# Optimization experiments

Measured on AMD Instinct MI355X. Metric: run time of the kernel, lower is better.

The kernel has to match this reference:

```python
import jax, jax.numpy as jnp
import numpy as np

DIM = 2048
NUM_SLOTS = 64
MEM_DIM = 512
TEMP = 0.1


def setup_inputs() -> dict:
    key = jax.random.key(0)
    k_x, k_mem, k_kp, k_vp, k_gw, k_gb = jax.random.split(key, 6)
    B, L = 8, 4096
    return {
        "x": jax.random.normal(k_x, (B, L, DIM), dtype=jnp.float32),
        "memory": jax.random.normal(k_mem, (NUM_SLOTS, MEM_DIM), dtype=jnp.float32),
        # torch Linear weight layout: [out_features, in_features]
        "key_w": jax.random.normal(k_kp, (MEM_DIM, DIM), dtype=jnp.float32) * (1.0 / np.sqrt(DIM)),
        "value_w": jax.random.normal(k_vp, (DIM, MEM_DIM), dtype=jnp.float32) * (1.0 / np.sqrt(MEM_DIM)),
        "gate_w": jax.random.normal(k_gw, (1, 2 * DIM), dtype=jnp.float32) * (1.0 / np.sqrt(2 * DIM)),
        "gate_b": jnp.zeros((1,), dtype=jnp.float32),
    }


def reference(x, memory, key_w, value_w, gate_w, gate_b):
    # query = key_proj(x): [B,L,mem_dim]
    query = jnp.einsum('bld,md->blm', x, key_w)
    # attention over memory slots: [B,L,num_slots]
    attn = jax.nn.softmax(jnp.einsum('blm,nm->bln', query, memory) / TEMP, axis=-1)
    # retrieve and project back to dim: [B,L,dim]
    retrieved = jnp.einsum('bln,nm->blm', attn, memory)
    retrieved = jnp.einsum('blm,dm->bld', retrieved, value_w)
    # gate from concat([x, retrieved]) -> Linear(2*dim, 1) -> sigmoid
    gate_logit = (jnp.einsum('bld,od->blo', x, gate_w[:, :DIM])
                  + jnp.einsum('bld,od->blo', retrieved, gate_w[:, DIM:])
                  + gate_b)
    gate = jax.nn.sigmoid(gate_logit)  # [B,L,1]
    return gate * x + (1.0 - gate) * retrieved
```

## Files before the change

### kernel.cpp

```cpp
#include <hip/hip_runtime.h>
#include <stdint.h>

#define DIM   2048
#define NSLOT 64
#define MDIM  512
#define TINV  10.0f

typedef __attribute__((ext_vector_type(4))) float     f32x4;
typedef __attribute__((ext_vector_type(8))) _Float16  half8;

#define MFMA16(a,b,c) __builtin_amdgcn_mfma_f32_16x16x32_f16((a),(b),(c),0,0,0)

#define OFF_W2F   0
#define OFF_W3T   1310720
#define OFF_H     1572864
#define OFF_TPART 1573120

__device__ __forceinline__ size_t w2f_idx(int row, int k, int lvl) {
    const int t  = row >> 4, ar = row & 15;
    const int ch = k >> 7, ks = (k >> 5) & 3, kg = (k >> 3) & 3, e = k & 7;
    return ((size_t)((((ch * 5 + t) * 4 + ks) * 2 + lvl) * 64) + kg * 16 + ar) * 8 + e;
}


__global__ __launch_bounds__(256) void prep_all(
    const float* __restrict__ memory, const float* __restrict__ key_w,
    const float* __restrict__ value_w, const float* __restrict__ gate_w,
    _Float16* __restrict__ W2F, _Float16* __restrict__ W3T,
    float* __restrict__ tpart)
{
    const int tid = threadIdx.x;
    const int c = blockIdx.x;
    const int role = blockIdx.y;

    if (role == 17) {
        const int b = c;
        float a0 = 0.f, a1 = 0.f;
        for (int d = b * 256; d < b * 256 + 256; ++d) {
            const float gv = gate_w[DIM + d];
            a0 = fmaf(value_w[(size_t)d * MDIM + tid], gv, a0);
            a1 = fmaf(value_w[(size_t)d * MDIM + tid + 256], gv, a1);
        }
        tpart[b * 512 + tid] = a0;
        tpart[b * 512 + tid + 256] = a1;
        return;
    }

    if (role < 9) {
        const int g = role;
        const int k = c * 256 + tid;
        if (g == 8) {
            float v = gate_w[k];
            _Float16 ph = (_Float16)v;
            _Float16 pl = (_Float16)(v - (float)ph);
            W2F[w2f_idx(64, k, 0)] = ph;
            W2F[w2f_idx(64, k, 1)] = pl;
            for (int r = 65; r < 80; ++r) {
                W2F[w2f_idx(r, k, 0)] = (_Float16)0.f;
                W2F[w2f_idx(r, k, 1)] = (_Float16)0.f;
            }
            return;
        }
        __shared__ __align__(16) float mem_s[8 * MDIM];
        for (int i = tid; i < 8 * MDIM; i += 256)
            mem_s[i] = memory[g * 8 * MDIM + i];
        __syncthreads();

        const f32x4* ms4 = (const f32x4*)mem_s;
        float acc[8] = {};
        for (int m4 = 0; m4 < MDIM / 4; ++m4) {
            const float kw0 = key_w[(size_t)(m4 * 4 + 0) * DIM + k];
            const float kw1 = key_w[(size_t)(m4 * 4 + 1) * DIM + k];
            const float kw2 = key_w[(size_t)(m4 * 4 + 2) * DIM + k];
            const float kw3 = key_w[(size_t)(m4 * 4 + 3) * DIM + k];
            #pragma unroll
            for (int i = 0; i < 8; ++i) {
                const f32x4 mv = ms4[i * (MDIM / 4) + m4];
                acc[i] = fmaf(mv.x, kw0, acc[i]);
                acc[i] = fmaf(mv.y, kw1, acc[i]);
                acc[i] = fmaf(mv.z, kw2, acc[i]);
                acc[i] = fmaf(mv.w, kw3, acc[i]);
            }
        }
        #pragma unroll
        for (int i = 0; i < 8; ++i) {
            float v = acc[i];
            _Float16 ph = (_Float16)v;
            _Float16 pl = (_Float16)(v - (float)ph);
            W2F[w2f_idx(g * 8 + i, k, 0)] = ph;
            W2F[w2f_idx(g * 8 + i, k, 1)] = pl;
        }
        return;
    }

    {
        const int g = role - 9;
        const int d = c * 256 + tid;
        __shared__ __align__(16) float mem_s2[8 * MDIM];
        for (int i = tid; i < 8 * MDIM; i += 256)
            mem_s2[i] = memory[g * 8 * MDIM + i];
        __syncthreads();

        const f32x4* ms4 = (const f32x4*)mem_s2;
        const f32x4* vp = (const f32x4*)(value_w + (size_t)d * MDIM);
        float acc[8] = {};
        for (int m4 = 0; m4 < MDIM / 4; ++m4) {
            const f32x4 v = vp[m4];
            #pragma unroll
            for (int i = 0; i < 8; ++i) {
                const f32x4 mv = ms4[i * (MDIM / 4) + m4];
                acc[i] = fmaf(mv.x, v.x, acc[i]);
                acc[i] = fmaf(mv.y, v.y, acc[i]);
                acc[i] = fmaf(mv.z, v.z, acc[i]);
                acc[i] = fmaf(mv.w, v.w, acc[i]);
            }
        }
        #pragma unroll
        for (int i = 0; i < 8; ++i)
            W3T[(size_t)d * NSLOT + g * 8 + i] = (_Float16)acc[i];
    }
}

__global__ __launch_bounds__(512) void prep_h(
    const float* __restrict__ memory, const float* __restrict__ tpart,
    float* __restrict__ h)
{
    __shared__ float ts[512];
    const int tid = threadIdx.x;
    float s = 0.f;
    #pragma unroll
    for (int b = 0; b < 8; ++b) s += tpart[b * 512 + tid];
    ts[tid] = s;
    __syncthreads();
    const int lane = tid & 63, w = tid >> 6;
    #pragma unroll
    for (int q = 0; q < 8; ++q) {
        const int n = w * 8 + q;
        float p = 0.f;
        for (int m = lane; m < MDIM; m += 64)
            p = fmaf(memory[(size_t)n * MDIM + m], ts[m], p);
        #pragma unroll
        for (int off = 32; off; off >>= 1) p += __shfl_xor(p, off);
        if (lane == 0) h[n] = p;
    }
}


__global__ __launch_bounds__(512, 4) void fused_kernel(
    const float* __restrict__ x,
    const _Float16* __restrict__ W2F,
    const _Float16* __restrict__ W3T,
    const float* __restrict__ h, const float* __restrict__ gate_b,
    float* __restrict__ out)
{
    __shared__ __align__(16) float ppart[4 * 5 * 64 * 4];
    __shared__ __align__(16) _Float16 attn_s[4][16][72];
    __shared__ float gate_s[4][16];

    const int tid  = threadIdx.x;
    const int lane = tid & 63;
    const int w    = tid >> 6;
    const int mt   = w & 3;
    const int kh   = w >> 2;
    const int arow = lane & 15;
    const int kg   = lane >> 4;
    const size_t row0 = (size_t)blockIdx.x * 64;

    f32x4 acc[5];
    {   f32x4 z = {0.f, 0.f, 0.f, 0.f};
        #pragma unroll
        for (int t = 0; t < 5; ++t) acc[t] = z; }

    const float* xrow = x + (row0 + mt * 16 + arow) * DIM + kg * 8;
    const _Float16* w2l8 = W2F + lane * 8;
    const int chbase = kh * 8;

    f32x4 xA[8], xB[8];
    auto load_x = [&](f32x4* X, int chn) {
        #pragma unroll
        for (int ks = 0; ks < 4; ++ks) {
            X[ks * 2]     = *(const f32x4*)(xrow + chn * 128 + ks * 32);
            X[ks * 2 + 1] = *(const f32x4*)(xrow + chn * 128 + ks * 32 + 4);
        }
    };
    auto compute_chunk = [&](const f32x4* X, int ch) {
        #pragma unroll
        for (int ks = 0; ks < 4; ++ks) {
            const f32x4 xa = X[ks * 2];
            const f32x4 xb = X[ks * 2 + 1];
            const float xf[8] = {xa.x, xa.y, xa.z, xa.w, xb.x, xb.y, xb.z, xb.w};
            _Float16 hh[8], ll[8];
            #pragma unroll
            for (int u = 0; u < 8; ++u) {
                hh[u] = (_Float16)xf[u];
                ll[u] = (_Float16)(xf[u] - (float)hh[u]);
            }
            const half8 ah = {hh[0], hh[1], hh[2], hh[3], hh[4], hh[5], hh[6], hh[7]};
            const half8 al = {ll[0], ll[1], ll[2], ll[3], ll[4], ll[5], ll[6], ll[7]};
            #pragma unroll
            for (int t = 0; t < 5; ++t) {
                const _Float16* p = w2l8 + (size_t)(((ch * 5 + t) * 4 + ks) * 2) * 512;
                const half8 bh = *(const half8*)p;
                const half8 bl = *(const half8*)(p + 512);
                acc[t] = MFMA16(ah, bh, acc[t]);
                acc[t] = MFMA16(al, bh, acc[t]);
                acc[t] = MFMA16(ah, bl, acc[t]);
            }
        }
    };

    load_x(xA, chbase);
    for (int cp = 0; cp < 8; cp += 2) {
        load_x(xB, chbase + cp + 1);
        compute_chunk(xA, chbase + cp);
        if (cp + 2 < 8) load_x(xA, chbase + cp + 2);
        compute_chunk(xB, chbase + cp + 1);
    }

    if (kh == 1) {
        #pragma unroll
        for (int t = 0; t < 5; ++t)
            *(f32x4*)(ppart + (size_t)((mt * 5 + t) * 64 + lane) * 4) = acc[t];
    }
    __syncthreads();

    if (kh == 0) {
        #pragma unroll
        for (int t = 0; t < 5; ++t)
            acc[t] += *(const f32x4*)(ppart + (size_t)((mt * 5 + t) * 64 + lane) * 4);

        float hl[4];
        #pragma unroll
        for (int t = 0; t < 4; ++t) hl[t] = h[t * 16 + arow];
        const float gb = gate_b[0];

        #pragma unroll
        for (int j = 0; j < 4; ++j) {
            float m = fmaxf(fmaxf(acc[0][j], acc[1][j]), fmaxf(acc[2][j], acc[3][j]));
            #pragma unroll
            for (int off = 1; off < 16; off <<= 1) m = fmaxf(m, __shfl_xor(m, off));
            float p[4];
            float sum = 0.f;
            #pragma unroll
            for (int t = 0; t < 4; ++t) { p[t] = __expf((acc[t][j] - m) * TINV); sum += p[t]; }
            #pragma unroll
            for (int off = 1; off < 16; off <<= 1) sum += __shfl_xor(sum, off);
            const float inv = 1.f / sum;
            float gp = 0.f;
            #pragma unroll
            for (int t = 0; t < 4; ++t) {
                const float a = p[t] * inv;
                attn_s[mt][kg * 4 + j][t * 16 + arow] = (_Float16)a;
                gp = fmaf(a, hl[t], gp);
            }
            #pragma unroll
            for (int off = 1; off < 16; off <<= 1) gp += __shfl_xor(gp, off);
            const float sg = __shfl(acc[4][j], lane & 48);
            if (arow == 0)
                gate_s[mt][kg * 4 + j] = 1.f / (1.f + __expf(-(sg + gp + gb)));
        }
    }
    __syncthreads();

    const size_t rbase = row0 + mt * 16;
    const half8 a0 = *(const half8*)(&attn_s[mt][arow][kg * 8]);
    const half8 a1 = *(const half8*)(&attn_s[mt][arow][kg * 8 + 32]);
    const float g = gate_s[mt][arow];

    const size_t rowoff = (rbase + arow) * DIM + kh * 1024 + kg * 4;
    const float* xp = x + rowoff;
    float* op = out + rowoff;
    const _Float16* w3base = W3T + (size_t)(kh * 1024 + arow) * NSLOT + kg * 8;

    half8 qb0[4], qb1[4];
    f32x4 qx[4];
    #pragma unroll
    for (int s = 0; s < 4; ++s) {
        const _Float16* bp = w3base + (size_t)s * 16 * NSLOT;
        qb0[s] = *(const half8*)bp;
        qb1[s] = *(const half8*)(bp + 32);
        qx[s]  = *(const f32x4*)(xp + s * 16);
    }

    #pragma unroll 4
    for (int dt = 0; dt < 64; ++dt) {
        const int s = dt & 3;
        f32x4 r = {0.f, 0.f, 0.f, 0.f};
        r = MFMA16(qb0[s], a0, r);
        r = MFMA16(qb1[s], a1, r);
        const f32x4 xv = qx[s];
        int nt = dt + 4; if (nt > 63) nt = 63;
        const _Float16* bp = w3base + (size_t)nt * 16 * NSLOT;
        qb0[s] = *(const half8*)bp;
        qb1[s] = *(const half8*)(bp + 32);
        qx[s]  = *(const f32x4*)(xp + (size_t)nt * 16);
        f32x4 o;
        o.x = fmaf(g, xv.x - r.x, r.x);
        o.y = fmaf(g, xv.y - r.y, r.y);
        o.z = fmaf(g, xv.z - r.z, r.z);
        o.w = fmaf(g, xv.w - r.w, r.w);
        *(f32x4*)(op + dt * 16) = o;
    }
}


extern "C" void kernel_launch(void* const* d_in, const int* in_sizes, int n_in,
                              void* d_out, int out_size, void* d_ws, size_t ws_size,
                              hipStream_t stream) {
    (void)in_sizes; (void)n_in; (void)out_size; (void)ws_size;
    const float* x       = (const float*)d_in[0];
    const float* memory  = (const float*)d_in[1];
    const float* key_w   = (const float*)d_in[2];
    const float* value_w = (const float*)d_in[3];
    const float* gate_w  = (const float*)d_in[4];
    const float* gate_b  = (const float*)d_in[5];
    float* out = (float*)d_out;

    char* wsb = (char*)d_ws;
    _Float16* W2F = (_Float16*)(wsb + OFF_W2F);
    _Float16* W3T = (_Float16*)(wsb + OFF_W3T);
    float*    h   = (float*)(wsb + OFF_H);
    float*    tpt = (float*)(wsb + OFF_TPART);

    prep_all<<<dim3(8, 18), 256, 0, stream>>>(memory, key_w, value_w, gate_w,
                                              W2F, W3T, tpt);
    prep_h  <<<1, 512, 0, stream>>>(memory, tpt, h);

    fused_kernel<<<512, 512, 0, stream>>>(x, W2F, W3T, h, gate_b, out);
}
```

Measured before the change: 301.5 us.

## Stage W2 chunks in LDS via async global_load_lds and split K by ks

```diff
diff --git a/kernel.cpp b/kernel.cpp
--- a/kernel.cpp
+++ b/kernel.cpp
@@ -153,6 +153,7 @@
     const float* __restrict__ h, const float* __restrict__ gate_b,
     float* __restrict__ out)
 {
+    __shared__ __align__(16) _Float16 w2s[20480];
     __shared__ __align__(16) float ppart[4 * 5 * 64 * 4];
     __shared__ __align__(16) _Float16 attn_s[4][16][72];
     __shared__ float gate_s[4][16];
@@ -172,22 +173,33 @@
         for (int t = 0; t < 5; ++t) acc[t] = z; }
 
     const float* xrow = x + (row0 + mt * 16 + arow) * DIM + kg * 8;
-    const _Float16* w2l8 = W2F + lane * 8;
-    const int chbase = kh * 8;
-
-    f32x4 xA[8], xB[8];
+
+    auto dma = [&](int ch) {
+        #pragma unroll
+        for (int i = 0; i < 5; ++i) {
+            const char* src = (const char*)W2F + (size_t)ch * 40960 + (size_t)(i * 512 + tid) * 16;
+            _Float16* dst = w2s + (size_t)(i * 512 + w * 64) * 8;
+            __builtin_amdgcn_global_load_lds(
+                (const __attribute__((address_space(1))) void*)src,
+                (__attribute__((address_space(3))) void*)dst, 16, 0, 0);
+        }
+    };
+
+    f32x4 xA[4], xB[4];
     auto load_x = [&](f32x4* X, int chn) {
         #pragma unroll
-        for (int ks = 0; ks < 4; ++ks) {
-            X[ks * 2]     = *(const f32x4*)(xrow + chn * 128 + ks * 32);
-            X[ks * 2 + 1] = *(const f32x4*)(xrow + chn * 128 + ks * 32 + 4);
+        for (int ksi = 0; ksi < 2; ++ksi) {
+            const int ks = kh * 2 + ksi;
+            X[ksi * 2]     = *(const f32x4*)(xrow + chn * 128 + ks * 32);
+            X[ksi * 2 + 1] = *(const f32x4*)(xrow + chn * 128 + ks * 32 + 4);
         }
     };
-    auto compute_chunk = [&](const f32x4* X, int ch) {
-        #pragma unroll
-        for (int ks = 0; ks < 4; ++ks) {
-            const f32x4 xa = X[ks * 2];
-            const f32x4 xb = X[ks * 2 + 1];
+    auto compute_chunk = [&](const f32x4* X) {
+        #pragma unroll
+        for (int ksi = 0; ksi < 2; ++ksi) {
+            const int ks = kh * 2 + ksi;
+            const f32x4 xa = X[ksi * 2];
+            const f32x4 xb = X[ksi * 2 + 1];
             const float xf[8] = {xa.x, xa.y, xa.z, xa.w, xb.x, xb.y, xb.z, xb.w};
             _Float16 hh[8], ll[8];
             #pragma unroll
@@ -199,7 +211,7 @@
             const half8 al = {ll[0], ll[1], ll[2], ll[3], ll[4], ll[5], ll[6], ll[7]};
             #pragma unroll
             for (int t = 0; t < 5; ++t) {
-                const _Float16* p = w2l8 + (size_t)(((ch * 5 + t) * 4 + ks) * 2) * 512;
+                const _Float16* p = w2s + (size_t)(t * 4 + ks) * 1024 + lane * 8;
                 const half8 bh = *(const half8*)p;
                 const half8 bl = *(const half8*)(p + 512);
                 acc[t] = MFMA16(ah, bh, acc[t]);
@@ -209,12 +221,27 @@
         }
     };
 
-    load_x(xA, chbase);
-    for (int cp = 0; cp < 8; cp += 2) {
-        load_x(xB, chbase + cp + 1);
-        compute_chunk(xA, chbase + cp);
-        if (cp + 2 < 8) load_x(xA, chbase + cp + 2);
-        compute_chunk(xB, chbase + cp + 1);
+    dma(0);
+    load_x(xA, 0);
+    #pragma unroll 1
+    for (int chp = 0; chp < 16; chp += 2) {
+        asm volatile("s_waitcnt vmcnt(0)" ::: "memory");
+        __builtin_amdgcn_s_barrier();
+        load_x(xB, chp + 1);
+        asm volatile("" ::: "memory");
+        compute_chunk(xA);
+        asm volatile("" ::: "memory");
+        __builtin_amdgcn_s_barrier();
+        dma(chp + 1);
+
+        asm volatile("s_waitcnt vmcnt(0)" ::: "memory");
+        __builtin_amdgcn_s_barrier();
+        if (chp + 2 < 16) load_x(xA, chp + 2);
+        asm volatile("" ::: "memory");
+        compute_chunk(xB);
+        asm volatile("" ::: "memory");
+        __builtin_amdgcn_s_barrier();
+        if (chp + 2 < 16) dma(chp + 2);
     }
 
     if (kh == 1) {
```

Result: faster. 282.3 us (-6.4%).

## Stage key-projection weights through LDS with async global_load_lds double buffering

Applied to the files above, without the earlier changes.

```diff
diff --git a/kernel.cpp b/kernel.cpp
--- a/kernel.cpp
+++ b/kernel.cpp
@@ -10,6 +10,8 @@
 typedef __attribute__((ext_vector_type(8))) _Float16  half8;
 
 #define MFMA16(a,b,c) __builtin_amdgcn_mfma_f32_16x16x32_f16((a),(b),(c),0,0,0)
+#define AS1 __attribute__((address_space(1)))
+#define AS3 __attribute__((address_space(3)))
 
 #define OFF_W2F   0
 #define OFF_W3T   1310720
@@ -18,8 +20,8 @@
 
 __device__ __forceinline__ size_t w2f_idx(int row, int k, int lvl) {
     const int t  = row >> 4, ar = row & 15;
-    const int ch = k >> 7, ks = (k >> 5) & 3, kg = (k >> 3) & 3, e = k & 7;
-    return ((size_t)((((ch * 5 + t) * 4 + ks) * 2 + lvl) * 64) + kg * 16 + ar) * 8 + e;
+    const int ch = k >> 6, ks = (k >> 5) & 1, kg = (k >> 3) & 3, e = k & 7;
+    return ((size_t)((((ch * 5 + t) * 2 + ks) * 2 + lvl) * 64) + kg * 16 + ar) * 8 + e;
 }
 
 
@@ -153,6 +155,7 @@
     const float* __restrict__ h, const float* __restrict__ gate_b,
     float* __restrict__ out)
 {
+    __shared__ __align__(16) _Float16 w2s[2][10240];
     __shared__ __align__(16) float ppart[4 * 5 * 64 * 4];
     __shared__ __align__(16) _Float16 attn_s[4][16][72];
     __shared__ float gate_s[4][16];
@@ -172,49 +175,67 @@
         for (int t = 0; t < 5; ++t) acc[t] = z; }
 
     const float* xrow = x + (row0 + mt * 16 + arow) * DIM + kg * 8;
-    const _Float16* w2l8 = W2F + lane * 8;
-    const int chbase = kh * 8;
-
-    f32x4 xA[8], xB[8];
-    auto load_x = [&](f32x4* X, int chn) {
-        #pragma unroll
-        for (int ks = 0; ks < 4; ++ks) {
-            X[ks * 2]     = *(const f32x4*)(xrow + chn * 128 + ks * 32);
-            X[ks * 2 + 1] = *(const f32x4*)(xrow + chn * 128 + ks * 32 + 4);
-        }
+
+    auto dma = [&](int ch, int buf) {
+        const char* base = (const char*)W2F + (size_t)ch * 20480;
+        _Float16* db = &w2s[buf][0];
+        __builtin_amdgcn_global_load_lds(
+            (const AS1 void*)(base + (size_t)tid * 16),
+            (AS3 void*)(db + (size_t)(w * 64) * 8), 16, 0, 0);
+        __builtin_amdgcn_global_load_lds(
+            (const AS1 void*)(base + (size_t)(512 + tid) * 16),
+            (AS3 void*)(db + (size_t)(512 + w * 64) * 8), 16, 0, 0);
+        if (w < 4)
+            __builtin_amdgcn_global_load_lds(
+                (const AS1 void*)(base + (size_t)(1024 + tid) * 16),
+                (AS3 void*)(db + (size_t)(1024 + w * 64) * 8), 16, 0, 0);
     };
-    auto compute_chunk = [&](const f32x4* X, int ch) {
-        #pragma unroll
-        for (int ks = 0; ks < 4; ++ks) {
-            const f32x4 xa = X[ks * 2];
-            const f32x4 xb = X[ks * 2 + 1];
-            const float xf[8] = {xa.x, xa.y, xa.z, xa.w, xb.x, xb.y, xb.z, xb.w};
-            _Float16 hh[8], ll[8];
-            #pragma unroll
-            for (int u = 0; u < 8; ++u) {
-                hh[u] = (_Float16)xf[u];
-                ll[u] = (_Float16)(xf[u] - (float)hh[u]);
-            }
-            const half8 ah = {hh[0], hh[1], hh[2], hh[3], hh[4], hh[5], hh[6], hh[7]};
-            const half8 al = {ll[0], ll[1], ll[2], ll[3], ll[4], ll[5], ll[6], ll[7]};
-            #pragma unroll
-            for (int t = 0; t < 5; ++t) {
-                const _Float16* p = w2l8 + (size_t)(((ch * 5 + t) * 4 + ks) * 2) * 512;
-                const half8 bh = *(const half8*)p;
-                const half8 bl = *(const half8*)(p + 512);
-                acc[t] = MFMA16(ah, bh, acc[t]);
-                acc[t] = MFMA16(al, bh, acc[t]);
-                acc[t] = MFMA16(ah, bl, acc[t]);
-            }
-        }
+
+    f32x4 xA[2], xB[2];
+    auto load_x = [&](f32x4* X, int ch) {
+        X[0] = *(const f32x4*)(xrow + ch * 64 + kh * 32);
+        X[1] = *(const f32x4*)(xrow + ch * 64 + kh * 32 + 4);
     };
-
-    load_x(xA, chbase);
-    for (int cp = 0; cp < 8; cp += 2) {
-        load_x(xB, chbase + cp + 1);
-        compute_chunk(xA, chbase + cp);
-        if (cp + 2 < 8) load_x(xA, chbase + cp + 2);
-        compute_chunk(xB, chbase + cp + 1);
+    auto compute_chunk = [&](const f32x4* X, int buf) {
+        const f32x4 xa = X[0];
+        const f32x4 xb = X[1];
+        const float xf[8] = {xa.x, xa.y, xa.z, xa.w, xb.x, xb.y, xb.z, xb.w};
+        _Float16 hh[8], ll[8];
+        #pragma unroll
+        for (int u = 0; u < 8; ++u) {
+            hh[u] = (_Float16)xf[u];
+            ll[u] = (_Float16)(xf[u] - (float)hh[u]);
+        }
+        const half8 ah = {hh[0], hh[1], hh[2], hh[3], hh[4], hh[5], hh[6], hh[7]};
+        const half8 al = {ll[0], ll[1], ll[2], ll[3], ll[4], ll[5], ll[6], ll[7]};
+        #pragma unroll
+        for (int t = 0; t < 5; ++t) {
+            const _Float16* p = &w2s[buf][0] + (size_t)((t * 2 + kh) * 2) * 512 + lane * 8;
+            const half8 bh = *(const half8*)p;
+            const half8 bl = *(const half8*)(p + 512);
+            acc[t] = MFMA16(ah, bh, acc[t]);
+            acc[t] = MFMA16(al, bh, acc[t]);
+            acc[t] = MFMA16(ah, bl, acc[t]);
+        }
+    };
+
+    dma(0, 0);
+    load_x(xA, 0);
+    dma(1, 1);
+    load_x(xB, 1);
+    #pragma unroll 2
+    for (int ch = 0; ch < 32; ++ch) {
+        if (ch < 31) asm volatile("s_waitcnt vmcnt(4)" ::: "memory");
+        else         asm volatile("s_waitcnt vmcnt(0)" ::: "memory");
+        __builtin_amdgcn_s_barrier();
+        asm volatile("" ::: "memory");
+        compute_chunk((ch & 1) ? xB : xA, ch & 1);
+        asm volatile("" ::: "memory");
+        __builtin_amdgcn_s_barrier();
+        if (ch + 2 < 32) {
+            dma(ch + 2, ch & 1);
+            load_x((ch & 1) ? xB : xA, ch + 2);
+        }
     }
 
     if (kh == 1) {
```

Result: faster. 278.3 us (-7.7%).

## Stage x and W2 chunks through LDS with async global_load_lds pipeline

Applied to the files above, without the earlier changes.

```diff
diff --git a/kernel.cpp b/kernel.cpp
--- a/kernel.cpp
+++ b/kernel.cpp
@@ -10,6 +10,8 @@
 typedef __attribute__((ext_vector_type(8))) _Float16  half8;
 
 #define MFMA16(a,b,c) __builtin_amdgcn_mfma_f32_16x16x32_f16((a),(b),(c),0,0,0)
+#define AS1 __attribute__((address_space(1)))
+#define AS3 __attribute__((address_space(3)))
 
 #define OFF_W2F   0
 #define OFF_W3T   1310720
@@ -18,8 +20,9 @@
 
 __device__ __forceinline__ size_t w2f_idx(int row, int k, int lvl) {
     const int t  = row >> 4, ar = row & 15;
-    const int ch = k >> 7, ks = (k >> 5) & 3, kg = (k >> 3) & 3, e = k & 7;
-    return ((size_t)((((ch * 5 + t) * 4 + ks) * 2 + lvl) * 64) + kg * 16 + ar) * 8 + e;
+    const int ch = k >> 6, ks = (k >> 5) & 1, kg = (k >> 3) & 3, e = k & 7;
+    return (size_t)ch * 12288 +
+           ((size_t)(((t * 2 + ks) * 2 + lvl) * 64) + kg * 16 + ar) * 8 + e;
 }
 
 
@@ -146,13 +149,15 @@
 }
 
 
-__global__ __launch_bounds__(512, 4) void fused_kernel(
+__global__ __launch_bounds__(512) void fused_kernel(
     const float* __restrict__ x,
     const _Float16* __restrict__ W2F,
     const _Float16* __restrict__ W3T,
     const float* __restrict__ h, const float* __restrict__ gate_b,
     float* __restrict__ out)
 {
+    __shared__ __align__(16) _Float16 w2s[2][12288];
+    __shared__ __align__(16) float    xs[4][4096];
     __shared__ __align__(16) float ppart[4 * 5 * 64 * 4];
     __shared__ __align__(16) _Float16 attn_s[4][16][72];
     __shared__ float gate_s[4][16];
@@ -171,50 +176,67 @@
         #pragma unroll
         for (int t = 0; t < 5; ++t) acc[t] = z; }
 
-    const float* xrow = x + (row0 + mt * 16 + arow) * DIM + kg * 8;
-    const _Float16* w2l8 = W2F + lane * 8;
-    const int chbase = kh * 8;
-
-    f32x4 xA[8], xB[8];
-    auto load_x = [&](f32x4* X, int chn) {
-        #pragma unroll
-        for (int ks = 0; ks < 4; ++ks) {
-            X[ks * 2]     = *(const f32x4*)(xrow + chn * 128 + ks * 32);
-            X[ks * 2 + 1] = *(const f32x4*)(xrow + chn * 128 + ks * 32 + 4);
-        }
+    auto dmaW2 = [&](int ch, int buf) {
+        const char* base = (const char*)W2F + (size_t)ch * 24576;
+        char* db = (char*)&w2s[buf][0];
+        #pragma unroll
+        for (int i = 0; i < 3; ++i)
+            __builtin_amdgcn_global_load_lds(
+                (const AS1 void*)(base + (size_t)(i * 512 + tid) * 16),
+                (AS3 void*)(db + (size_t)(i * 512 + w * 64) * 16), 16, 0, 0);
     };
-    auto compute_chunk = [&](const f32x4* X, int ch) {
-        #pragma unroll
-        for (int ks = 0; ks < 4; ++ks) {
-            const f32x4 xa = X[ks * 2];
-            const f32x4 xb = X[ks * 2 + 1];
-            const float xf[8] = {xa.x, xa.y, xa.z, xa.w, xb.x, xb.y, xb.z, xb.w};
-            _Float16 hh[8], ll[8];
-            #pragma unroll
-            for (int u = 0; u < 8; ++u) {
-                hh[u] = (_Float16)xf[u];
-                ll[u] = (_Float16)(xf[u] - (float)hh[u]);
-            }
-            const half8 ah = {hh[0], hh[1], hh[2], hh[3], hh[4], hh[5], hh[6], hh[7]};
-            const half8 al = {ll[0], ll[1], ll[2], ll[3], ll[4], ll[5], ll[6], ll[7]};
-            #pragma unroll
-            for (int t = 0; t < 5; ++t) {
-                const _Float16* p = w2l8 + (size_t)(((ch * 5 + t) * 4 + ks) * 2) * 512;
-                const half8 bh = *(const half8*)p;
-                const half8 bl = *(const half8*)(p + 512);
-                acc[t] = MFMA16(ah, bh, acc[t]);
-                acc[t] = MFMA16(al, bh, acc[t]);
-                acc[t] = MFMA16(ah, bl, acc[t]);
-            }
+    auto dmaX = [&](int ch, int buf) {
+        char* db = (char*)&xs[buf][0];
+        #pragma unroll
+        for (int i = 0; i < 2; ++i) {
+            const int gid = i * 512 + tid;
+            const int row = gid >> 4, gq = gid & 15;
+            const char* src = (const char*)(x + (size_t)(row0 + row) * DIM + ch * 64)
+                              + ((gq ^ (row & 7)) << 4);
+            __builtin_amdgcn_global_load_lds(
+                (const AS1 void*)src,
+                (AS3 void*)(db + (size_t)(i * 512 + w * 64) * 16), 16, 0, 0);
         }
     };
 
-    load_x(xA, chbase);
-    for (int cp = 0; cp < 8; cp += 2) {
-        load_x(xB, chbase + cp + 1);
-        compute_chunk(xA, chbase + cp);
-        if (cp + 2 < 8) load_x(xA, chbase + cp + 2);
-        compute_chunk(xB, chbase + cp + 1);
+    auto compute_chunk = [&](int xbuf, int wbuf) {
+        const int row = mt * 16 + arow;
+        const char* xrb = (const char*)&xs[xbuf][0] + row * 256;
+        const int g0 = kh * 8 + kg * 2;
+        const f32x4 xa = *(const f32x4*)(xrb + ((g0 ^ (arow & 7)) << 4));
+        const f32x4 xb = *(const f32x4*)(xrb + (((g0 + 1) ^ (arow & 7)) << 4));
+        const float xf[8] = {xa.x, xa.y, xa.z, xa.w, xb.x, xb.y, xb.z, xb.w};
+        _Float16 hh[8], ll[8];
+        #pragma unroll
+        for (int u = 0; u < 8; ++u) {
+            hh[u] = (_Float16)xf[u];
+            ll[u] = (_Float16)(xf[u] - (float)hh[u]);
+        }
+        const half8 ah = {hh[0], hh[1], hh[2], hh[3], hh[4], hh[5], hh[6], hh[7]};
+        const half8 al = {ll[0], ll[1], ll[2], ll[3], ll[4], ll[5], ll[6], ll[7]};
+        #pragma unroll
+        for (int t = 0; t < 5; ++t) {
+            const _Float16* p = &w2s[wbuf][0] + (size_t)((t * 2 + kh) * 2) * 512 + lane * 8;
+            const half8 bh = *(const half8*)p;
+            const half8 bl = *(const half8*)(p + 512);
+            acc[t] = MFMA16(ah, bh, acc[t]);
+            acc[t] = MFMA16(al, bh, acc[t]);
+            acc[t] = MFMA16(ah, bl, acc[t]);
+        }
+    };
+
+    dmaW2(0, 0); dmaX(0, 0);
+    dmaW2(1, 1); dmaX(1, 1);
+    dmaX(2, 2);  dmaX(3, 3);
+    #pragma unroll 4
+    for (int ch = 0; ch < 32; ++ch) {
+        if (ch < 28) asm volatile("s_waitcnt vmcnt(7)" ::: "memory");
+        else         asm volatile("s_waitcnt vmcnt(0)" ::: "memory");
+        __builtin_amdgcn_s_barrier();
+        compute_chunk(ch & 3, ch & 1);
+        __builtin_amdgcn_s_barrier();
+        if (ch + 2 < 32) dmaW2(ch + 2, ch & 1);
+        if (ch + 4 < 32) dmaX(ch + 4, ch & 3);
     }
 
     if (kh == 1) {
```

New measurement: 267.0 us. 11.5% less time.
